# Kernel tuning notes

Hardware: AMD Instinct MI355X
Metric: run time of the kernel (lower is better)

Reference implementation:

```python
import jax, jax.numpy as jnp
import numpy as np

# DeepSeek V4 MLA sparse attention dims
T = 512            # query tokens
H = 64             # attention heads (SUPPORTED_HEAD_COUNTS)
KV_LORA = 512      # kv_lora_rank (value dim = latent nope part)
ROPE = 64          # qk_rope_head_dim
D = KV_LORA + ROPE # 576 = head_dim (matches alignment=576 in cache spec)
N_KV = 8192        # cached compressed-KV tokens
TOPK = 1024        # top-k selected tokens per query
SCALE = 1.0 / np.sqrt(D).astype(np.float32)


def setup_inputs() -> dict:
    key = jax.random.key(0)
    k1, k2, k3, k4 = jax.random.split(key, 4)
    q = jax.random.normal(k1, (T, H, D), dtype=jnp.float32)
    kv = jax.random.normal(k2, (N_KV, D), dtype=jnp.float32)   # compressed KV latent cache (1 kv head)
    topk_idx = jax.random.randint(k3, (T, TOPK), 0, N_KV, dtype=jnp.int32)
    sink = jax.random.normal(k4, (H,), dtype=jnp.float32)       # per-head attention sink logit
    return {"q": q, "kv": kv, "topk_idx": topk_idx, "sink": sink}


def reference(q, kv, topk_idx, sink):
    # Sparse MLA: each query token attends only to its top-k latent cache slots.
    valid = topk_idx >= 0                       # invalid slots marked negative
    idx = jnp.maximum(topk_idx, 0)
    g = kv[idx]                                  # [T, K, D] gathered latents
    # scores over gathered subset: [T, H, K]
    scores = jnp.einsum('thd,tkd->thk', q, g) * SCALE
    scores = jnp.where(valid[:, None, :], scores, -jnp.inf)
    # sink-aware softmax: sink acts as an extra logit with zero value
    m = jnp.maximum(jnp.max(scores, axis=-1), sink[None, :])   # [T, H]
    p = jnp.exp(scores - m[..., None])                          # [T, H, K]
    denom = jnp.sum(p, axis=-1) + jnp.exp(sink[None, :] - m)    # [T, H]
    # value = nope part (first KV_LORA dims) of latent -> output [T, H, KV_LORA]
    out = jnp.einsum('thk,tkv->thv', p, g[..., :KV_LORA]) / denom[..., None]
    return out
```

## Files before the change

kernel.cpp:

```cpp
#include <hip/hip_runtime.h>
#include <hip/hip_bf16.h>

#define T_TOK 512
#define NH    64
#define HD    576
#define DVAL  512
#define NKV   8192
#define TOPK  1024
#define KT    32
#define NITER (TOPK / KT)
#define SCALE 0.041666666666666664f
#define LOG2E 1.4426950408889634f
#define QSCL  (SCALE * LOG2E)
#define MFIX  8.0f
#define MB    (MFIX * LOG2E)

typedef __attribute__((ext_vector_type(4))) float f32x4;
typedef __attribute__((ext_vector_type(8))) _Float16 half8;
typedef __attribute__((ext_vector_type(4))) unsigned short us4;
typedef __attribute__((ext_vector_type(8))) unsigned short us8;
typedef __attribute__((ext_vector_type(4))) int i32x4;

__device__ __forceinline__ unsigned short f2h(float x) {
    _Float16 h = (_Float16)x;
    return __builtin_bit_cast(unsigned short, h);
}

__device__ __forceinline__ float fexp2(float x) {
#if __has_builtin(__builtin_amdgcn_exp2f)
    return __builtin_amdgcn_exp2f(x);
#else
    return __expf(x * 0.6931471805599453f);
#endif
}

template<int CTRL>
__device__ __forceinline__ float dppmv(float x) {
    int r = __builtin_amdgcn_update_dpp(0, __builtin_bit_cast(int, x), CTRL, 0xF, 0xF, true);
    return __builtin_bit_cast(float, r);
}
__device__ __forceinline__ float red16sum(float x) {
    x += dppmv<0xB1>(x);
    x += dppmv<0x4E>(x);
    x += dppmv<0x141>(x);
    x += dppmv<0x140>(x);
    return x;
}

#define TICK_BARRIER() do {                                   \
    asm volatile("s_waitcnt lgkmcnt(0)" ::: "memory");        \
    __builtin_amdgcn_s_barrier();                             \
    asm volatile("" ::: "memory");                            \
} while (0)

#if __has_builtin(__builtin_amdgcn_global_load_lds)
#define HAVE_GLOAD 1
#define GLOAD16(src, ldsbase)                                              \
    __builtin_amdgcn_global_load_lds(                                      \
        (const __attribute__((address_space(1))) void*)(src),              \
        (__attribute__((address_space(3))) void*)(ldsbase), 16, 0, 0)
#else
#define HAVE_GLOAD 0
#endif

__global__ void cvt_kv_f16(const float* __restrict__ kv, unsigned short* __restrict__ kvb) {
    int i = blockIdx.x * 256 + threadIdx.x;
    const f32x4* src = (const f32x4*)kv + (size_t)i * 2;
    f32x4 a = src[0];
    f32x4 b = src[1];
    us8 w;
    w[0]=f2h(a[0]); w[1]=f2h(a[1]); w[2]=f2h(a[2]); w[3]=f2h(a[3]);
    w[4]=f2h(b[0]); w[5]=f2h(b[1]); w[6]=f2h(b[2]); w[7]=f2h(b[3]);
    ((us8*)kvb)[i] = w;
}

#define P_LD  40
#define GT_IDX(row,key) (((((row) << 5) | (key))) ^ ((((row) >> 2) & 7) << 3))

struct StageRegs { us8 v[4]; };

__device__ __forceinline__ void stage_gload(
    const unsigned short* __restrict__ kvb, const int* __restrict__ tkrow,
    int it, int w8, int lane, unsigned short* g2d, unsigned short* roped)
{
#if HAVE_GLOAD
    #pragma unroll
    for (int j = 0; j < 4; j++) {
        int key = w8 * 4 + j;
        int row = tkrow[it * KT + key]; row = row < 0 ? 0 : row;
        int chunk = lane ^ (key & 7);
        GLOAD16(kvb + (size_t)row * HD + chunk * 8, g2d + key * 512);
    }
    if (w8 < 4) {
        int key = w8 * 8 + (lane >> 3);
        int row = tkrow[it * KT + key]; row = row < 0 ? 0 : row;
        int chunk = (lane & 7) ^ (key & 7);
        GLOAD16(kvb + (size_t)row * HD + 512 + chunk * 8, roped + w8 * 512);
    }
#else
    #pragma unroll
    for (int j = 0; j < 4; j++) {
        int key = w8 * 4 + j;
        int row = tkrow[it * KT + key]; row = row < 0 ? 0 : row;
        int chunk = lane ^ (key & 7);
        *(us8*)&g2d[key * 512 + lane * 8] =
            *(const us8*)(kvb + (size_t)row * HD + chunk * 8);
    }
    if (w8 < 4) {
        int key = w8 * 8 + (lane >> 3);
        int row = tkrow[it * KT + key]; row = row < 0 ? 0 : row;
        int chunk = (lane & 7) ^ (key & 7);
        *(us8*)&roped[w8 * 512 + lane * 8] =
            *(const us8*)(kvb + (size_t)row * HD + 512 + chunk * 8);
    }
#endif
}

__device__ __forceinline__ void stage_load(
    const unsigned short* __restrict__ kvb, const int* __restrict__ tkrow,
    int it, int w8, int kg, int lm, StageRegs& R)
{
    const int* ip = tkrow + it * KT + kg * 4;
    i32x4 r4 = *(const i32x4*)ip;
    int d0 = w8 * 64 + lm * 8;
    #pragma unroll
    for (int j = 0; j < 4; j++) {
        int r = r4[j] < 0 ? 0 : r4[j];
        R.v[j] = *(const us8*)(kvb + (size_t)r * HD + d0);
    }
}

__device__ __forceinline__ void stage_write_gt(
    int w8, int kg, int lm, const StageRegs& R, unsigned short* gtp)
{
    int d0 = w8 * 64 + lm * 8;
    #pragma unroll
    for (int e = 0; e < 8; e++) {
        us4 wv;
        wv[0] = R.v[0][e]; wv[1] = R.v[1][e]; wv[2] = R.v[2][e]; wv[3] = R.v[3][e];
        *(us4*)&gtp[GT_IDX(d0 + e, kg * 4)] = wv;
    }
}

__device__ __forceinline__ void pv_tick(
    int tau, const unsigned short* __restrict__ kvb, const int* __restrict__ tkrow,
    int w8, int kg, int lm, int quad, int l16, int lane, int col0,
    StageRegs& Lset, StageRegs& Wset,
    unsigned short* g2d_next, unsigned short* roped_next, unsigned short* gtp,
    const unsigned short (*pb)[P_LD],
    f32x4 (&acc)[4][4])
{
    const bool do_next  = (tau + 1 < NITER);
    const bool do_load2 = (tau + 2 < NITER);
    if (do_next)
        stage_gload(kvb, tkrow, tau + 1, w8, lane, g2d_next, roped_next);
    if (do_load2)
        stage_load(kvb, tkrow, tau + 2, w8, kg, lm, Lset);

    half8 pa[4];
    #pragma unroll
    for (int mt = 0; mt < 4; mt++)
        pa[mt] = *(const half8*)&pb[mt * 16 + l16][quad * 8];

    __builtin_amdgcn_s_setprio(1);
    #pragma unroll
    for (int nt = 0; nt < 4; nt++) {
        half8 vb = *(const half8*)&gtp[GT_IDX(col0 + nt * 16 + l16, quad * 8)];
        #pragma unroll
        for (int mt = 0; mt < 4; mt++)
            acc[mt][nt] = __builtin_amdgcn_mfma_f32_16x16x32_f16(pa[mt], vb, acc[mt][nt], 0, 0, 0);
    }
    __builtin_amdgcn_s_setprio(0);

    asm volatile("s_waitcnt lgkmcnt(0)" ::: "memory");
    if (do_next) {
        stage_write_gt(w8, kg, lm, Wset, gtp);
        if (do_load2) asm volatile("s_waitcnt vmcnt(4)" ::: "memory");
        else          asm volatile("s_waitcnt vmcnt(0)" ::: "memory");
    }
}

__global__ __launch_bounds__(768, 3) void mla_sparse_kernel(
    const float* __restrict__ q, const int* __restrict__ topk,
    const float* __restrict__ sink, const unsigned short* __restrict__ kvb,
    float* __restrict__ out)
{
    __shared__ unsigned short g2s[2][KT * 512];
    __shared__ unsigned short ropes[2][KT * 64];
    __shared__ unsigned short gtb[2][DVAL * KT];
    __shared__ unsigned short pbuf[2][NH][P_LD];
    __shared__ float lrunL[NH];

    const int tid  = threadIdx.x;
    const int lane = tid & 63;
    const int quad = lane >> 4;
    const int l16  = lane & 15;
    const int wave = __builtin_amdgcn_readfirstlane(tid >> 6);
    const int t    = blockIdx.x;
    const int* tkrow = topk + (size_t)t * TOPK;

    if (wave < 4) {
        const int w  = wave;
        const int qo = quad * 8;
        half8 qf[18];
        {
            const float* qrow = q + ((size_t)t * NH + (w * 16 + l16)) * HD;
            #pragma unroll
            for (int ks = 0; ks < 18; ks++) {
                int d0 = ks * 32 + qo;
                f32x4 a = *(const f32x4*)(qrow + d0);
                f32x4 b = *(const f32x4*)(qrow + d0 + 4);
                half8 h;
                h[0]=(_Float16)(a[0]*QSCL); h[1]=(_Float16)(a[1]*QSCL);
                h[2]=(_Float16)(a[2]*QSCL); h[3]=(_Float16)(a[3]*QSCL);
                h[4]=(_Float16)(b[0]*QSCL); h[5]=(_Float16)(b[1]*QSCL);
                h[6]=(_Float16)(b[2]*QSCL); h[7]=(_Float16)(b[3]*QSCL);
                qf[ks] = h;
            }
        }
        unsigned mb0 = 0, mb1 = 0;
        #pragma unroll 4
        for (int kk = 0; kk < NITER; kk++) {
            mb0 |= (tkrow[kk * KT + l16]      < 0) ? (1u << kk) : 0u;
            mb1 |= (tkrow[kk * KT + 16 + l16] < 0) ? (1u << kk) : 0u;
        }
        const int k7    = l16 & 7;
        const int sidx0 = l16 * 512 + ((quad ^ k7) << 3);
        const int sidx1 = l16 * 512 + (((4 + quad) ^ k7) << 3);
        const int ridx0 = l16 * 64 + ((quad ^ k7) << 3);
        const int ridx1 = l16 * 64 + (((4 + quad) ^ k7) << 3);
        f32x4 sk = *(const f32x4*)(sink + w * 16 + quad * 4);
        float l_part[4];
        #pragma unroll
        for (int r = 0; r < 4; r++)
            l_part[r] = (l16 == 0) ? fexp2(sk[r] * LOG2E - MB) : 0.0f;
        const int hb = w * 16 + quad * 4;

        __syncthreads();

        for (int k = 0; k <= NITER; k++) {
            if (k < NITER) {
                const int par = k & 1;
                const unsigned short* gp = g2s[par];
                const unsigned short* rp = ropes[par];
                f32x4 zero = {0.f, 0.f, 0.f, 0.f};
                f32x4 mbase = {-MB, -MB, -MB, -MB};
                f32x4 s0a = mbase, s0b = zero, s1a = mbase, s1b = zero;
                __builtin_amdgcn_s_setprio(1);
                #pragma unroll
                for (int ks = 0; ks < 16; ks += 2) {
                    int o = (ks >> 1) * 64;
                    half8 b0 = *(const half8*)&gp[sidx0 + o];
                    half8 b1 = *(const half8*)&gp[sidx0 + 8192 + o];
                    s0a = __builtin_amdgcn_mfma_f32_16x16x32_f16(qf[ks], b0, s0a, 0, 0, 0);
                    s1a = __builtin_amdgcn_mfma_f32_16x16x32_f16(qf[ks], b1, s1a, 0, 0, 0);
                    half8 c0 = *(const half8*)&gp[sidx1 + o];
                    half8 c1 = *(const half8*)&gp[sidx1 + 8192 + o];
                    s0b = __builtin_amdgcn_mfma_f32_16x16x32_f16(qf[ks+1], c0, s0b, 0, 0, 0);
                    s1b = __builtin_amdgcn_mfma_f32_16x16x32_f16(qf[ks+1], c1, s1b, 0, 0, 0);
                }
                {
                    half8 r0 = *(const half8*)&rp[ridx0];
                    half8 r1 = *(const half8*)&rp[ridx0 + 1024];
                    s0a = __builtin_amdgcn_mfma_f32_16x16x32_f16(qf[16], r0, s0a, 0, 0, 0);
                    s1a = __builtin_amdgcn_mfma_f32_16x16x32_f16(qf[16], r1, s1a, 0, 0, 0);
                    half8 r2 = *(const half8*)&rp[ridx1];
                    half8 r3 = *(const half8*)&rp[ridx1 + 1024];
                    s0b = __builtin_amdgcn_mfma_f32_16x16x32_f16(qf[17], r2, s0b, 0, 0, 0);
                    s1b = __builtin_amdgcn_mfma_f32_16x16x32_f16(qf[17], r3, s1b, 0, 0, 0);
                }
                __builtin_amdgcn_s_setprio(0);
                f32x4 s0 = s0a + s0b, s1 = s1a + s1b;
                const bool bad0 = (mb0 >> k) & 1;
                const bool bad1 = (mb1 >> k) & 1;
                const float NEG = -__builtin_inff();
                #pragma unroll
                for (int r = 0; r < 4; r++) {
                    float v0 = bad0 ? NEG : s0[r];
                    float v1 = bad1 ? NEG : s1[r];
                    float p0 = fexp2(v0);
                    float p1 = fexp2(v1);
                    l_part[r] += p0 + p1;
                    pbuf[par][hb + r][l16]      = f2h(p0);
                    pbuf[par][hb + r][16 + l16] = f2h(p1);
                }
            }
            TICK_BARRIER();
        }
        #pragma unroll
        for (int r = 0; r < 4; r++) l_part[r] = red16sum(l_part[r]);
        if (l16 == 0) {
            f32x4 l4; l4[0]=l_part[0]; l4[1]=l_part[1]; l4[2]=l_part[2]; l4[3]=l_part[3];
            *(f32x4*)&lrunL[hb] = l4;
        }
        __syncthreads();
    } else {
        const int w8   = wave - 4;
        const int col0 = w8 * 64;
        const int kg   = lane >> 3;
        const int lm   = lane & 7;
        f32x4 acc[4][4];
        f32x4 zero = {0.f, 0.f, 0.f, 0.f};
        #pragma unroll
        for (int mt = 0; mt < 4; mt++)
            #pragma unroll
            for (int nt = 0; nt < 4; nt++) acc[mt][nt] = zero;

        StageRegs A, B;
        stage_gload(kvb, tkrow, 0, w8, lane, g2s[0], ropes[0]);
        stage_load(kvb, tkrow, 0, w8, kg, lm, A);
        stage_write_gt(w8, kg, lm, A, gtb[0]);
        stage_load(kvb, tkrow, 1, w8, kg, lm, B);
        asm volatile("s_waitcnt vmcnt(4)" ::: "memory");
        __syncthreads();

        stage_gload(kvb, tkrow, 1, w8, lane, g2s[1], ropes[1]);
        stage_load(kvb, tkrow, 2, w8, kg, lm, A);
        asm volatile("s_waitcnt lgkmcnt(0)" ::: "memory");
        stage_write_gt(w8, kg, lm, B, gtb[1]);
        asm volatile("s_waitcnt vmcnt(4)" ::: "memory");
        TICK_BARRIER();

        for (int k = 1; k < NITER; k += 2) {
            pv_tick(k, kvb, tkrow, w8, kg, lm, quad, l16, lane, col0,
                    B, A, g2s[0], ropes[0], gtb[0], pbuf[0], acc);
            TICK_BARRIER();
            pv_tick(k + 1, kvb, tkrow, w8, kg, lm, quad, l16, lane, col0,
                    A, B, g2s[1], ropes[1], gtb[1], pbuf[1], acc);
            TICK_BARRIER();
        }
        __syncthreads();

        #pragma unroll
        for (int mt = 0; mt < 4; mt++) {
            f32x4 lv = *(const f32x4*)&lrunL[mt * 16 + quad * 4];
            f32x4 li;
            li[0] = 1.0f / lv[0]; li[1] = 1.0f / lv[1];
            li[2] = 1.0f / lv[2]; li[3] = 1.0f / lv[3];
            #pragma unroll
            for (int nt = 0; nt < 4; nt++) {
                int vcol = col0 + nt * 16 + l16;
                f32x4 r = acc[mt][nt] * li;
                #pragma unroll
                for (int rr = 0; rr < 4; rr++) {
                    int head = mt * 16 + quad * 4 + rr;
                    out[((size_t)t * NH + head) * DVAL + vcol] = r[rr];
                }
            }
        }
    }
}

extern "C" void kernel_launch(void* const* d_in, const int* in_sizes, int n_in,
                              void* d_out, int out_size, void* d_ws, size_t ws_size,
                              hipStream_t stream) {
    const float* q    = (const float*)d_in[0];
    const float* kv   = (const float*)d_in[1];
    const int*   topk = (const int*)d_in[2];
    const float* sink = (const float*)d_in[3];
    float* out = (float*)d_out;
    unsigned short* kvb = (unsigned short*)d_ws;

    cvt_kv_f16<<<NKV * HD / (256 * 8), 256, 0, stream>>>(kv, kvb);
    mla_sparse_kernel<<<T_TOK, 768, 0, stream>>>(q, topk, sink, kvb, out);
}
```

Baseline: 258.0 us.

## Split QK score computation across waves by head-dim halves with 32x32 MFMA and deeper pipeline

The four score waves now each cover 32 heads and half of the 576-wide head dimension, using 32x32x16 MFMAs instead of 16x16x32. Partial scores from the second half are handed to the first via global scratch in the output buffer, and softmax finalization is delayed by one tick. The PV waves' staging pipeline is reshuffled so the score and PV stages run one tick offset. This aims to balance the score work and overlap it better with PV, at the cost of extra scratch traffic, vmcnt waits and more complex synchronization.

```diff
diff --git a/kernel.cpp b/kernel.cpp
--- a/kernel.cpp
+++ b/kernel.cpp
@@ -14,8 +14,10 @@
 #define QSCL  (SCALE * LOG2E)
 #define MFIX  8.0f
 #define MB    (MFIX * LOG2E)
+#define P_LD  40
 
 typedef __attribute__((ext_vector_type(4))) float f32x4;
+typedef __attribute__((ext_vector_type(16))) float f32x16;
 typedef __attribute__((ext_vector_type(8))) _Float16 half8;
 typedef __attribute__((ext_vector_type(4))) unsigned short us4;
 typedef __attribute__((ext_vector_type(8))) unsigned short us8;
@@ -34,19 +36,6 @@
 #endif
 }
 
-template<int CTRL>
-__device__ __forceinline__ float dppmv(float x) {
-    int r = __builtin_amdgcn_update_dpp(0, __builtin_bit_cast(int, x), CTRL, 0xF, 0xF, true);
-    return __builtin_bit_cast(float, r);
-}
-__device__ __forceinline__ float red16sum(float x) {
-    x += dppmv<0xB1>(x);
-    x += dppmv<0x4E>(x);
-    x += dppmv<0x141>(x);
-    x += dppmv<0x140>(x);
-    return x;
-}
-
 #define TICK_BARRIER() do {                                   \
     asm volatile("s_waitcnt lgkmcnt(0)" ::: "memory");        \
     __builtin_amdgcn_s_barrier();                             \
@@ -54,11 +43,11 @@
 } while (0)
 
 #if __has_builtin(__builtin_amdgcn_global_load_lds)
-#define HAVE_GLOAD 1
 #define GLOAD16(src, ldsbase)                                              \
     __builtin_amdgcn_global_load_lds(                                      \
         (const __attribute__((address_space(1))) void*)(src),              \
         (__attribute__((address_space(3))) void*)(ldsbase), 16, 0, 0)
+#define HAVE_GLOAD 1
 #else
 #define HAVE_GLOAD 0
 #endif
@@ -74,7 +63,6 @@
     ((us8*)kvb)[i] = w;
 }
 
-#define P_LD  40
 #define GT_IDX(row,key) (((((row) << 5) | (key))) ^ ((((row) >> 2) & 7) << 3))
 
 struct StageRegs { us8 v[4]; };
@@ -116,7 +104,7 @@
 #endif
 }
 
-__device__ __forceinline__ void stage_load(
+__device__ __forceinline__ void stage_vload(
     const unsigned short* __restrict__ kvb, const int* __restrict__ tkrow,
     int it, int w8, int kg, int lm, StageRegs& R)
 {
@@ -142,42 +130,114 @@
     }
 }
 
+template<int PAR>
+__device__ __forceinline__ void s_tick(
+    int tau, int kh, int hg, int key, int kgrp, int k7, int lane,
+    const half8* qf, unsigned mbit,
+    const unsigned short* g2sp, const unsigned short* ropesp,
+    unsigned short (*pbuf_w)[P_LD],
+    float* scratch, float* l_den,
+    f32x16& Cs_save, f32x16& Cs_use)
+{
+    const bool fin = (kh == 0) && (tau >= 1) && (tau <= NITER);
+    f32x4 pr0, pr1, pr2, pr3;
+    if (fin) {
+        const float* prd = scratch + (hg * 2 + (PAR ^ 1)) * 1024 + lane * 4;
+        pr0 = *(const f32x4*)(prd);
+        pr1 = *(const f32x4*)(prd + 256);
+        pr2 = *(const f32x4*)(prd + 512);
+        pr3 = *(const f32x4*)(prd + 768);
+    }
+    f32x16 c;
+    #pragma unroll
+    for (int r = 0; r < 16; r++) c[r] = (kh == 0) ? -MB : 0.0f;
+    if (tau < NITER) {
+        __builtin_amdgcn_s_setprio(1);
+        if (kh == 0) {
+            #pragma unroll
+            for (int ks = 0; ks < 18; ks++) {
+                int cch = ks * 2 + kgrp;
+                half8 bf = *(const half8*)&g2sp[key * 512 + ((cch ^ k7) << 3)];
+                c = __builtin_amdgcn_mfma_f32_32x32x16_f16(qf[ks], bf, c, 0, 0, 0);
+            }
+        } else {
+            #pragma unroll
+            for (int ks = 0; ks < 14; ks++) {
+                int cch = 36 + ks * 2 + kgrp;
+                half8 bf = *(const half8*)&g2sp[key * 512 + ((cch ^ k7) << 3)];
+                c = __builtin_amdgcn_mfma_f32_32x32x16_f16(qf[ks], bf, c, 0, 0, 0);
+            }
+            #pragma unroll
+            for (int ks = 14; ks < 18; ks++) {
+                int cch = (ks - 14) * 2 + kgrp;
+                half8 bf = *(const half8*)&ropesp[key * 64 + ((cch ^ k7) << 3)];
+                c = __builtin_amdgcn_mfma_f32_32x32x16_f16(qf[ks], bf, c, 0, 0, 0);
+            }
+        }
+        __builtin_amdgcn_s_setprio(0);
+    }
+    if (fin) {
+        const bool bad = (mbit >> (tau - 1)) & 1;
+        #pragma unroll
+        for (int r = 0; r < 16; r++) {
+            float pv = (r < 4) ? pr0[r] : (r < 8) ? pr1[r - 4]
+                     : (r < 12) ? pr2[r - 8] : pr3[r - 12];
+            float s = Cs_use[r] + pv;
+            float p = bad ? 0.0f : fexp2(s);
+            l_den[r] += p;
+            int rowo = (r & 3) + 8 * (r >> 2) + 4 * kgrp;
+            pbuf_w[hg * 32 + rowo][key] = f2h(p);
+        }
+    }
+    if (kh == 1 && tau < NITER) {
+        float* pw = scratch + (hg * 2 + PAR) * 1024 + lane * 4;
+        *(f32x4*)(pw)       = __builtin_shufflevector(c, c, 0, 1, 2, 3);
+        *(f32x4*)(pw + 256) = __builtin_shufflevector(c, c, 4, 5, 6, 7);
+        *(f32x4*)(pw + 512) = __builtin_shufflevector(c, c, 8, 9, 10, 11);
+        *(f32x4*)(pw + 768) = __builtin_shufflevector(c, c, 12, 13, 14, 15);
+        asm volatile("s_waitcnt vmcnt(0)" ::: "memory");
+    }
+    Cs_save = c;
+}
+
+template<int PAR>
 __device__ __forceinline__ void pv_tick(
     int tau, const unsigned short* __restrict__ kvb, const int* __restrict__ tkrow,
     int w8, int kg, int lm, int quad, int l16, int lane, int col0,
     StageRegs& Lset, StageRegs& Wset,
-    unsigned short* g2d_next, unsigned short* roped_next, unsigned short* gtp,
+    unsigned short* g2_dst, unsigned short* rope_dst,
+    unsigned short* gt_w, const unsigned short* gt_r,
     const unsigned short (*pb)[P_LD],
     f32x4 (&acc)[4][4])
 {
-    const bool do_next  = (tau + 1 < NITER);
-    const bool do_load2 = (tau + 2 < NITER);
-    if (do_next)
-        stage_gload(kvb, tkrow, tau + 1, w8, lane, g2d_next, roped_next);
-    if (do_load2)
-        stage_load(kvb, tkrow, tau + 2, w8, kg, lm, Lset);
-
-    half8 pa[4];
-    #pragma unroll
-    for (int mt = 0; mt < 4; mt++)
-        pa[mt] = *(const half8*)&pb[mt * 16 + l16][quad * 8];
-
-    __builtin_amdgcn_s_setprio(1);
-    #pragma unroll
-    for (int nt = 0; nt < 4; nt++) {
-        half8 vb = *(const half8*)&gtp[GT_IDX(col0 + nt * 16 + l16, quad * 8)];
+    if (tau + 1 < NITER)
+        stage_gload(kvb, tkrow, tau + 1, w8, lane, g2_dst, rope_dst);
+    if (tau < NITER)
+        stage_vload(kvb, tkrow, tau, w8, kg, lm, Lset);
+
+    if (tau >= 2) {
+        half8 pa[4];
         #pragma unroll
         for (int mt = 0; mt < 4; mt++)
-            acc[mt][nt] = __builtin_amdgcn_mfma_f32_16x16x32_f16(pa[mt], vb, acc[mt][nt], 0, 0, 0);
-    }
-    __builtin_amdgcn_s_setprio(0);
-
-    asm volatile("s_waitcnt lgkmcnt(0)" ::: "memory");
-    if (do_next) {
-        stage_write_gt(w8, kg, lm, Wset, gtp);
-        if (do_load2) asm volatile("s_waitcnt vmcnt(4)" ::: "memory");
-        else          asm volatile("s_waitcnt vmcnt(0)" ::: "memory");
-    }
+            pa[mt] = *(const half8*)&pb[mt * 16 + l16][quad * 8];
+        __builtin_amdgcn_s_setprio(1);
+        #pragma unroll
+        for (int nt = 0; nt < 4; nt++) {
+            half8 vb = *(const half8*)&gt_r[GT_IDX(col0 + nt * 16 + l16, quad * 8)];
+            #pragma unroll
+            for (int mt = 0; mt < 4; mt++)
+                acc[mt][nt] = __builtin_amdgcn_mfma_f32_16x16x32_f16(pa[mt], vb, acc[mt][nt], 0, 0, 0);
+        }
+        __builtin_amdgcn_s_setprio(0);
+    }
+    if (tau >= 1 && tau <= NITER) {
+        if (tau + 1 < NITER)      { asm volatile("s_waitcnt vmcnt(8)" ::: "memory"); }
+        else if (tau < NITER)     { asm volatile("s_waitcnt vmcnt(4)" ::: "memory"); }
+        else                      { asm volatile("s_waitcnt vmcnt(0)" ::: "memory"); }
+        stage_write_gt(w8, kg, lm, Wset, gt_w);
+    }
+    if (tau + 1 < NITER)
+        asm volatile("s_waitcnt vmcnt(4)" ::: "memory");
 }
 
 __global__ __launch_bounds__(768, 3) void mla_sparse_kernel(
@@ -198,16 +258,20 @@
     const int wave = __builtin_amdgcn_readfirstlane(tid >> 6);
     const int t    = blockIdx.x;
     const int* tkrow = topk + (size_t)t * TOPK;
+    float* scratch = out + (size_t)t * (NH * DVAL);
 
     if (wave < 4) {
-        const int w  = wave;
-        const int qo = quad * 8;
+        const int kh   = wave >> 1;
+        const int hg   = wave & 1;
+        const int key  = lane & 31;
+        const int kgrp = lane >> 5;
+        const int k7   = lane & 7;
         half8 qf[18];
         {
-            const float* qrow = q + ((size_t)t * NH + (w * 16 + l16)) * HD;
+            const float* qrow = q + ((size_t)t * NH + hg * 32 + key) * HD + kh * 288;
             #pragma unroll
             for (int ks = 0; ks < 18; ks++) {
-                int d0 = ks * 32 + qo;
+                int d0 = ks * 16 + kgrp * 8;
                 f32x4 a = *(const f32x4*)(qrow + d0);
                 f32x4 b = *(const f32x4*)(qrow + d0 + 4);
                 half8 h;
@@ -218,80 +282,43 @@
                 qf[ks] = h;
             }
         }
-        unsigned mb0 = 0, mb1 = 0;
-        #pragma unroll 4
-        for (int kk = 0; kk < NITER; kk++) {
-            mb0 |= (tkrow[kk * KT + l16]      < 0) ? (1u << kk) : 0u;
-            mb1 |= (tkrow[kk * KT + 16 + l16] < 0) ? (1u << kk) : 0u;
-        }
-        const int k7    = l16 & 7;
-        const int sidx0 = l16 * 512 + ((quad ^ k7) << 3);
-        const int sidx1 = l16 * 512 + (((4 + quad) ^ k7) << 3);
-        const int ridx0 = l16 * 64 + ((quad ^ k7) << 3);
-        const int ridx1 = l16 * 64 + (((4 + quad) ^ k7) << 3);
-        f32x4 sk = *(const f32x4*)(sink + w * 16 + quad * 4);
-        float l_part[4];
-        #pragma unroll
-        for (int r = 0; r < 4; r++)
-            l_part[r] = (l16 == 0) ? fexp2(sk[r] * LOG2E - MB) : 0.0f;
-        const int hb = w * 16 + quad * 4;
+        unsigned mbit = 0;
+        if (kh == 0) {
+            #pragma unroll 4
+            for (int kk = 0; kk < NITER; kk++)
+                mbit |= (tkrow[kk * KT + key] < 0) ? (1u << kk) : 0u;
+        }
+        float l_den[16];
+        #pragma unroll
+        for (int r = 0; r < 16; r++) {
+            if (kh == 0 && key == 0) {
+                int head = hg * 32 + (r & 3) + 8 * (r >> 2) + 4 * kgrp;
+                l_den[r] = fexp2(sink[head] * LOG2E - MB);
+            } else {
+                l_den[r] = 0.0f;
+            }
+        }
+        f32x16 CsA, CsB;
 
         __syncthreads();
 
-        for (int k = 0; k <= NITER; k++) {
-            if (k < NITER) {
-                const int par = k & 1;
-                const unsigned short* gp = g2s[par];
-                const unsigned short* rp = ropes[par];
-                f32x4 zero = {0.f, 0.f, 0.f, 0.f};
-                f32x4 mbase = {-MB, -MB, -MB, -MB};
-                f32x4 s0a = mbase, s0b = zero, s1a = mbase, s1b = zero;
-                __builtin_amdgcn_s_setprio(1);
-                #pragma unroll
-                for (int ks = 0; ks < 16; ks += 2) {
-                    int o = (ks >> 1) * 64;
-                    half8 b0 = *(const half8*)&gp[sidx0 + o];
-                    half8 b1 = *(const half8*)&gp[sidx0 + 8192 + o];
-                    s0a = __builtin_amdgcn_mfma_f32_16x16x32_f16(qf[ks], b0, s0a, 0, 0, 0);
-                    s1a = __builtin_amdgcn_mfma_f32_16x16x32_f16(qf[ks], b1, s1a, 0, 0, 0);
-                    half8 c0 = *(const half8*)&gp[sidx1 + o];
-                    half8 c1 = *(const half8*)&gp[sidx1 + 8192 + o];
-                    s0b = __builtin_amdgcn_mfma_f32_16x16x32_f16(qf[ks+1], c0, s0b, 0, 0, 0);
-                    s1b = __builtin_amdgcn_mfma_f32_16x16x32_f16(qf[ks+1], c1, s1b, 0, 0, 0);
-                }
-                {
-                    half8 r0 = *(const half8*)&rp[ridx0];
-                    half8 r1 = *(const half8*)&rp[ridx0 + 1024];
-                    s0a = __builtin_amdgcn_mfma_f32_16x16x32_f16(qf[16], r0, s0a, 0, 0, 0);
-                    s1a = __builtin_amdgcn_mfma_f32_16x16x32_f16(qf[16], r1, s1a, 0, 0, 0);
-                    half8 r2 = *(const half8*)&rp[ridx1];
-                    half8 r3 = *(const half8*)&rp[ridx1 + 1024];
-                    s0b = __builtin_amdgcn_mfma_f32_16x16x32_f16(qf[17], r2, s0b, 0, 0, 0);
-                    s1b = __builtin_amdgcn_mfma_f32_16x16x32_f16(qf[17], r3, s1b, 0, 0, 0);
-                }
-                __builtin_amdgcn_s_setprio(0);
-                f32x4 s0 = s0a + s0b, s1 = s1a + s1b;
-                const bool bad0 = (mb0 >> k) & 1;
-                const bool bad1 = (mb1 >> k) & 1;
-                const float NEG = -__builtin_inff();
-                #pragma unroll
-                for (int r = 0; r < 4; r++) {
-                    float v0 = bad0 ? NEG : s0[r];
-                    float v1 = bad1 ? NEG : s1[r];
-                    float p0 = fexp2(v0);
-                    float p1 = fexp2(v1);
-                    l_part[r] += p0 + p1;
-                    pbuf[par][hb + r][l16]      = f2h(p0);
-                    pbuf[par][hb + r][16 + l16] = f2h(p1);
-                }
-            }
+        for (int k = 0; k < NITER + 2; k += 2) {
+            s_tick<0>(k, kh, hg, key, kgrp, k7, lane, qf, mbit,
+                      g2s[0], ropes[0], pbuf[1], scratch, l_den, CsA, CsB);
             TICK_BARRIER();
-        }
-        #pragma unroll
-        for (int r = 0; r < 4; r++) l_part[r] = red16sum(l_part[r]);
-        if (l16 == 0) {
-            f32x4 l4; l4[0]=l_part[0]; l4[1]=l_part[1]; l4[2]=l_part[2]; l4[3]=l_part[3];
-            *(f32x4*)&lrunL[hb] = l4;
+            s_tick<1>(k + 1, kh, hg, key, kgrp, k7, lane, qf, mbit,
+                      g2s[1], ropes[1], pbuf[0], scratch, l_den, CsB, CsA);
+            TICK_BARRIER();
+        }
+        if (kh == 0) {
+            #pragma unroll
+            for (int r = 0; r < 16; r++) {
+                float v = l_den[r];
+                v += __shfl_xor(v, 1); v += __shfl_xor(v, 2); v += __shfl_xor(v, 4);
+                v += __shfl_xor(v, 8); v += __shfl_xor(v, 16);
+                if (key == 0)
+                    lrunL[hg * 32 + (r & 3) + 8 * (r >> 2) + 4 * kgrp] = v;
+            }
         }
         __syncthreads();
     } else {
@@ -308,25 +335,15 @@
 
         StageRegs A, B;
         stage_gload(kvb, tkrow, 0, w8, lane, g2s[0], ropes[0]);
-        stage_load(kvb, tkrow, 0, w8, kg, lm, A);
-        stage_write_gt(w8, kg, lm, A, gtb[0]);
-        stage_load(kvb, tkrow, 1, w8, kg, lm, B);
-        asm volatile("s_waitcnt vmcnt(4)" ::: "memory");
+        asm volatile("s_waitcnt vmcnt(0)" ::: "memory");
         __syncthreads();
 
-        stage_gload(kvb, tkrow, 1, w8, lane, g2s[1], ropes[1]);
-        stage_load(kvb, tkrow, 2, w8, kg, lm, A);
-        asm volatile("s_waitcnt lgkmcnt(0)" ::: "memory");
-        stage_write_gt(w8, kg, lm, B, gtb[1]);
-        asm volatile("s_waitcnt vmcnt(4)" ::: "memory");
-        TICK_BARRIER();
-
-        for (int k = 1; k < NITER; k += 2) {
-            pv_tick(k, kvb, tkrow, w8, kg, lm, quad, l16, lane, col0,
-                    B, A, g2s[0], ropes[0], gtb[0], pbuf[0], acc);
+        for (int k = 0; k < NITER + 2; k += 2) {
+            pv_tick<0>(k, kvb, tkrow, w8, kg, lm, quad, l16, lane, col0,
+                       A, B, g2s[1], ropes[1], gtb[1], gtb[0], pbuf[0], acc);
             TICK_BARRIER();
-            pv_tick(k + 1, kvb, tkrow, w8, kg, lm, quad, l16, lane, col0,
-                    A, B, g2s[1], ropes[1], gtb[1], pbuf[1], acc);
+            pv_tick<1>(k + 1, kvb, tkrow, w8, kg, lm, quad, l16, lane, col0,
+                       B, A, g2s[0], ropes[0], gtb[0], gtb[1], pbuf[1], acc);
             TICK_BARRIER();
         }
         __syncthreads();
```

Measured after the change: 429.7 us. +66.5%, slower.
